# Kernel optimization log

Hardware: AMD Instinct MI355X
Metric: run time of the kernel (lower is better)

Reference implementation:

```python
import jax, jax.numpy as jnp
import numpy as np

SUB_NO = 128
T_HIST = 100
T_DATA = 20000
SYN_B = 3
HIST_B = 3
FIX_VAR = 1.0


def _build_kern(delta, log_tau, K):
    # delta: (S,), log_tau: (B,), K: (S,B) -> kernel (S, T_HIST)
    t = jnp.maximum(jnp.arange(T_HIST, dtype=jnp.float32)[None, :] - delta[:, None], 0.0)  # (S,T)
    tt = t[:, :, None] / jnp.exp(log_tau)[None, None, :]  # (S,T,B)
    return jnp.einsum('stb,sb->st', tt * jnp.exp(-tt), K)


def setup_inputs() -> dict:
    key = jax.random.key(0)
    ks = jax.random.split(key, 5)
    S = SUB_NO
    return {
        'S_conv': jax.random.normal(ks[0], (T_DATA, S), jnp.float32),
        'Y_ancest': jax.random.normal(ks[1], (T_DATA, S), jnp.float32),
        'Z_ancest': jax.random.uniform(ks[2], (T_DATA, S), jnp.float32),
        'noise': jax.random.normal(ks[3], (T_DATA, S), jnp.float32),
        'C_den': jax.random.uniform(ks[4], (S, S), jnp.float32),
        'W_sub': jnp.ones(S, jnp.float32) * 0.25,
        'theta_syn': jnp.zeros(S, jnp.float32),
        'K_spike': jnp.ones((S, SYN_B), jnp.float32) * 0.01,
        'tau_spike': jnp.arange(1.6, 1.6 + SYN_B, dtype=jnp.float32),
        'delta_spike': jnp.zeros(S, jnp.float32),
        'theta_spike': jnp.ones(S, jnp.float32) * (-1.0),
        'W_spike': jnp.ones(S, jnp.float32) * 0.1,
        'tau_hist': jnp.arange(0.5, 0.5 + HIST_B * 0.5, 0.5, dtype=jnp.float32),
        'K_hist': jnp.zeros((S, HIST_B), jnp.float32),
        'delta_hist': jnp.zeros(S, jnp.float32),
    }


def _forward(S_conv, Y_ancest, Z_ancest, noise, C_den, W_sub, theta_syn,
             K_spike, tau_spike, delta_spike, theta_spike, W_spike,
             tau_hist, K_hist, delta_hist):
    S = SUB_NO
    # kernels, flipped as in torch (conv1d cross-correlation with flipped kernel)
    hist_kf = _build_kern(delta_hist, tau_hist, K_hist)[:, ::-1]      # (S,T_HIST)
    anc_kf = _build_kern(delta_spike, tau_spike, K_spike)[:, ::-1]    # (S,T_HIST)

    # Ancestor path has no recurrence -> hoist out of the time loop.
    # spike_ancest filtering: C_den is linear & time-independent, so project first,
    # then depthwise-convolve along time.
    Z_pad = jnp.concatenate([jnp.zeros((T_HIST, S), S_conv.dtype), Z_ancest], axis=0)  # (T+T_HIST,S)
    A = Z_pad @ C_den.T  # (T+T_HIST, S)
    conv = jax.lax.conv_general_dilated(
        A.T[None],                 # (1, S, T+T_HIST)
        anc_kf[:, None, :],        # (S, 1, T_HIST)
        window_strides=(1,), padding='VALID',
        dimension_numbers=('NCH', 'OIH', 'NCH'),
        feature_group_count=S)     # (1, S, T_DATA+1)
    filtered_ancest = conv[0].T[:T_DATA]  # (T_DATA, S)

    raw_ancest = Y_ancest @ C_den.T  # (T_DATA, S)
    base = S_conv + theta_syn + filtered_ancest + raw_ancest  # (T_DATA,S)
    sqrt_var = FIX_VAR ** 0.5

    def step(buf, inp):
        # buf: (S, T_HIST) rolling history of Z_out (most recent at index -1)
        b, n = inp
        fh = jnp.sum(buf * hist_kf, axis=1)            # grouped conv1d == per-channel dot
        x_out = jax.nn.sigmoid(b + fh)
        down = x_out * W_spike + theta_spike           # down_mu_Z_t == mu_Z_t (up_mu_Z=None)
        z_out = jax.nn.sigmoid(down + n * sqrt_var)
        buf = jnp.concatenate([buf[:, 1:], z_out[:, None]], axis=1)
        return buf, (x_out * W_sub, z_out, down)

    buf0 = jnp.zeros((S, T_HIST), S_conv.dtype)
    _, (final_Y, final_Z, mu_Z) = jax.lax.scan(step, buf0, (base, noise))
    return final_Y, final_Z, mu_Z, mu_Z


def reference(S_conv, Y_ancest, Z_ancest, noise, C_den, W_sub, theta_syn,
              K_spike, tau_spike, delta_spike, theta_spike, W_spike,
              tau_hist, K_hist, delta_hist):
    return _forward(S_conv, Y_ancest, Z_ancest, noise, C_den, W_sub, theta_syn,
                    K_spike, tau_spike, delta_spike, theta_spike, W_spike,
                    tau_hist, K_hist, delta_hist)
```

## Files before the change

kernel.cpp:

```cpp
#include <hip/hip_runtime.h>

#define T_DATA 20000
#define S_NO   128
#define T_HIST 100
#define NELEM  (T_DATA * S_NO)

__device__ __forceinline__ float sigm(float v) {
    return 1.0f / (1.0f + __expf(-v));
}

__global__ void k1_prep(const float* __restrict__ C,
                        const float* __restrict__ K_spike,
                        const float* __restrict__ tau_spike,
                        const float* __restrict__ delta_spike,
                        const float* __restrict__ tau_hist,
                        const float* __restrict__ K_hist,
                        const float* __restrict__ delta_hist,
                        float* __restrict__ Ct,
                        float* __restrict__ anc_kT,
                        float* __restrict__ hist_k,
                        int* __restrict__ flag) {
    const int tid = threadIdx.x;
    for (int q = tid; q < S_NO * S_NO; q += 256) {
        int s = q >> 7, k = q & 127;
        Ct[k * S_NO + s] = C[q];
    }
    const int s    = tid & 127;
    const int half = tid >> 7;
    {
        float d  = delta_spike[s];
        float i0 = __expf(-tau_spike[0]);
        float i1 = __expf(-tau_spike[1]);
        float i2 = __expf(-tau_spike[2]);
        float k0 = K_spike[s * 3 + 0], k1 = K_spike[s * 3 + 1], k2 = K_spike[s * 3 + 2];
        for (int j = half * 50; j < half * 50 + 50; ++j) {
            float t  = fmaxf((float)j - d, 0.0f);
            float x0 = t * i0, x1 = t * i1, x2 = t * i2;
            anc_kT[j * S_NO + s] =
                k0 * x0 * __expf(-x0) + k1 * x1 * __expf(-x1) + k2 * x2 * __expf(-x2);
        }
    }
    {
        float d  = delta_hist[s];
        float i0 = __expf(-tau_hist[0]);
        float i1 = __expf(-tau_hist[1]);
        float i2 = __expf(-tau_hist[2]);
        float k0 = K_hist[s * 3 + 0], k1 = K_hist[s * 3 + 1], k2 = K_hist[s * 3 + 2];
        for (int j = half * 50; j < half * 50 + 50; ++j) {
            float t  = fmaxf((float)j - d, 0.0f);
            float x0 = t * i0, x1 = t * i1, x2 = t * i2;
            hist_k[s * T_HIST + j] =
                k0 * x0 * __expf(-x0) + k1 * x1 * __expf(-x1) + k2 * x2 * __expf(-x2);
        }
    }
    if (tid == 0) *flag = 0;
    __syncthreads();
    if (tid < 128) {
        if (K_hist[s * 3] != 0.0f || K_hist[s * 3 + 1] != 0.0f || K_hist[s * 3 + 2] != 0.0f)
            atomicOr(flag, 1);
    }
}

__global__ void __launch_bounds__(256) k2_gemm(const float* __restrict__ Z,
                                               const float* __restrict__ Y,
                                               const float* __restrict__ Ct,
                                               float* __restrict__ A,
                                               float* __restrict__ R) {
    __shared__ float Zt[16][128];
    __shared__ float Yt[16][128];
    const int t0  = blockIdx.x * 16;
    const int tid = threadIdx.x;
    {
        const float4* Zg = (const float4*)(Z + t0 * S_NO);
        const float4* Yg = (const float4*)(Y + t0 * S_NO);
        float4* Zl = (float4*)&Zt[0][0];
        float4* Yl = (float4*)&Yt[0][0];
        for (int q = tid; q < 512; q += 256) { Zl[q] = Zg[q]; Yl[q] = Yg[q]; }
    }
    __syncthreads();
    const int s  = tid & 127;
    const int tb = (tid >> 7) * 8;
    float accA[8] = {0, 0, 0, 0, 0, 0, 0, 0};
    float accR[8] = {0, 0, 0, 0, 0, 0, 0, 0};
    for (int k4 = 0; k4 < 32; ++k4) {
        const float c0 = Ct[(k4 * 4 + 0) * S_NO + s];
        const float c1 = Ct[(k4 * 4 + 1) * S_NO + s];
        const float c2 = Ct[(k4 * 4 + 2) * S_NO + s];
        const float c3 = Ct[(k4 * 4 + 3) * S_NO + s];
#pragma unroll
        for (int i = 0; i < 8; ++i) {
            float4 z = *(const float4*)&Zt[tb + i][k4 * 4];
            accA[i] = fmaf(c0, z.x, fmaf(c1, z.y, fmaf(c2, z.z, fmaf(c3, z.w, accA[i]))));
            float4 y = *(const float4*)&Yt[tb + i][k4 * 4];
            accR[i] = fmaf(c0, y.x, fmaf(c1, y.y, fmaf(c2, y.z, fmaf(c3, y.w, accR[i]))));
        }
    }
#pragma unroll
    for (int i = 0; i < 8; ++i) {
        A[(t0 + tb + i) * S_NO + s] = accA[i];
        R[(t0 + tb + i) * S_NO + s] = accR[i];
    }
}

__global__ void __launch_bounds__(256) k3_conv(const float* __restrict__ A,
                                               const float* __restrict__ anc_kT,
                                               float* __restrict__ F) {
    __shared__ float Al[140 * 64];
    const int tstart = blockIdx.x * 40;
    const int shalf  = blockIdx.y;
    const int tid    = threadIdx.x;
    for (int q = tid; q < 140 * 16; q += 256) {
        const int row = q >> 4, c4 = q & 15;
        const int u  = tstart - 100 + row;
        float4 v = make_float4(0.f, 0.f, 0.f, 0.f);
        if (u >= 0) v = *(const float4*)&A[u * S_NO + shalf * 64 + c4 * 4];
        *(float4*)&Al[row * 64 + c4 * 4] = v;
    }
    __syncthreads();
    const int sl    = tid & 63;
    const int tg    = tid >> 6;
    const int sg    = shalf * 64 + sl;
    const int rbase = tg * 10;
    float acc[10] = {0, 0, 0, 0, 0, 0, 0, 0, 0, 0};
    float W[10];
#pragma unroll
    for (int i = 0; i < 10; ++i) W[i] = Al[(rbase + 99 + i) * 64 + sl];
#pragma unroll
    for (int j = 0; j < 100; ++j) {
        const float kv = anc_kT[j * S_NO + sg];
#pragma unroll
        for (int i = 0; i < 10; ++i)
            acc[i] = fmaf(W[(((i - j) % 10) + 10) % 10], kv, acc[i]);
        if (j < 99)
            W[(10 - ((j + 1) % 10)) % 10] = Al[(rbase + 98 - j) * 64 + sl];
    }
    const int T0 = tstart + rbase;
#pragma unroll
    for (int i = 0; i < 10; ++i) F[(T0 + i) * S_NO + sg] = acc[i];
}

__global__ void __launch_bounds__(256) k4_final(const float* __restrict__ S_conv,
                                                const float* __restrict__ noise,
                                                const float* __restrict__ W_sub,
                                                const float* __restrict__ theta_syn,
                                                const float* __restrict__ theta_spike,
                                                const float* __restrict__ W_spike,
                                                const float* __restrict__ hist_k,
                                                const int* __restrict__ flag,
                                                float* out0, float* out1,
                                                float* out2, float* out3) {
    __shared__ float zr[128];
    if (*flag == 0) {
        const int n4 = blockIdx.x * blockDim.x + threadIdx.x;
        if (n4 >= NELEM / 4) return;
        const int r = n4 & 31;
        const float4 sc = ((const float4*)S_conv)[n4];
        const float4 rr = ((const float4*)out1)[n4];
        const float4 ff = ((const float4*)out3)[n4];
        const float4 nz = ((const float4*)noise)[n4];
        const float4 ts = ((const float4*)theta_syn)[r];
        const float4 wu = ((const float4*)W_sub)[r];
        const float4 wk = ((const float4*)W_spike)[r];
        const float4 tk = ((const float4*)theta_spike)[r];
        float4 y, z, dn;
        {
            float x = sigm(sc.x + ts.x + rr.x + ff.x);
            y.x = x * wu.x; dn.x = fmaf(x, wk.x, tk.x); z.x = sigm(dn.x + nz.x);
        }
        {
            float x = sigm(sc.y + ts.y + rr.y + ff.y);
            y.y = x * wu.y; dn.y = fmaf(x, wk.y, tk.y); z.y = sigm(dn.y + nz.y);
        }
        {
            float x = sigm(sc.z + ts.z + rr.z + ff.z);
            y.z = x * wu.z; dn.z = fmaf(x, wk.z, tk.z); z.z = sigm(dn.z + nz.z);
        }
        {
            float x = sigm(sc.w + ts.w + rr.w + ff.w);
            y.w = x * wu.w; dn.w = fmaf(x, wk.w, tk.w); z.w = sigm(dn.w + nz.w);
        }
        ((float4*)out0)[n4] = y;
        ((float4*)out1)[n4] = z;
        ((float4*)out2)[n4] = dn;
        ((float4*)out3)[n4] = dn;
    } else {
        const int s = blockIdx.x;
        if (s >= S_NO || threadIdx.x >= 64) return;
        const int l = threadIdx.x;
        zr[l] = 0.0f; zr[l + 64] = 0.0f;
        const float hk0 = (l < T_HIST) ? hist_k[s * T_HIST + l] : 0.0f;
        const float hk1 = (l + 64 < T_HIST) ? hist_k[s * T_HIST + l + 64] : 0.0f;
        const float tsy = theta_syn[s], wsub = W_sub[s];
        const float wsp = W_spike[s],  tsp  = theta_spike[s];
        for (int t = 0; t < T_DATA; ++t) {
            float fh = hk0 * zr[(t - 1 - l) & 127];
            fh = fmaf(hk1, zr[(t - 65 - l) & 127], fh);
#pragma unroll
            for (int m = 1; m < 64; m <<= 1) fh += __shfl_xor(fh, m, 64);
            const int n = t * S_NO + s;
            const float basev = S_conv[n] + tsy + out1[n] + out3[n];
            const float x  = sigm(basev + fh);
            const float dn = fmaf(x, wsp, tsp);
            const float z  = sigm(dn + noise[n]);
            if (l == 0) {
                out0[n] = x * wsub;
                out1[n] = z;
                out2[n] = dn;
                out3[n] = dn;
                zr[t & 127] = z;
            }
        }
    }
}

extern "C" void kernel_launch(void* const* d_in, const int* in_sizes, int n_in,
                              void* d_out, int out_size, void* d_ws, size_t ws_size,
                              hipStream_t stream) {
    const float* S_conv  = (const float*)d_in[0];
    const float* Y_anc   = (const float*)d_in[1];
    const float* Z_anc   = (const float*)d_in[2];
    const float* noise   = (const float*)d_in[3];
    const float* C_den   = (const float*)d_in[4];
    const float* W_sub   = (const float*)d_in[5];
    const float* th_syn  = (const float*)d_in[6];
    const float* K_spk   = (const float*)d_in[7];
    const float* tau_spk = (const float*)d_in[8];
    const float* dl_spk  = (const float*)d_in[9];
    const float* th_spk  = (const float*)d_in[10];
    const float* W_spk   = (const float*)d_in[11];
    const float* tau_h   = (const float*)d_in[12];
    const float* K_h     = (const float*)d_in[13];
    const float* dl_h    = (const float*)d_in[14];

    float* out  = (float*)d_out;
    float* out0 = out;
    float* out1 = out + NELEM;
    float* out2 = out + 2 * NELEM;
    float* out3 = out + 3 * NELEM;

    float* ws      = (float*)d_ws;
    float* Ct      = ws;
    float* anc_kT  = ws + 16384;
    float* hist_k  = ws + 16384 + 12800;
    int*   flag    = (int*)(ws + 16384 + 25600);

    k1_prep<<<1, 256, 0, stream>>>(C_den, K_spk, tau_spk, dl_spk, tau_h, K_h, dl_h,
                                   Ct, anc_kT, hist_k, flag);
    k2_gemm<<<T_DATA / 16, 256, 0, stream>>>(Z_anc, Y_anc, Ct, out0, out1);
    k3_conv<<<dim3(T_DATA / 40, 2), 256, 0, stream>>>(out0, anc_kT, out3);
    k4_final<<<(NELEM / 4 + 255) / 256, 256, 0, stream>>>(S_conv, noise, W_sub, th_syn,
                                                          th_spk, W_spk, hist_k, flag,
                                                          out0, out1, out2, out3);
}
```

Measured before the change: 189.4 us.

## Fuse ancestor convolution with elementwise output stage and parallelize prep transpose

```diff
diff --git a/kernel.cpp b/kernel.cpp
--- a/kernel.cpp
+++ b/kernel.cpp
@@ -9,7 +9,7 @@
     return 1.0f / (1.0f + __expf(-v));
 }
 
-__global__ void k1_prep(const float* __restrict__ C,
+__global__ void __launch_bounds__(256) k1_prep(const float* __restrict__ C,
                         const float* __restrict__ K_spike,
                         const float* __restrict__ tau_spike,
                         const float* __restrict__ delta_spike,
@@ -21,9 +21,14 @@
                         float* __restrict__ hist_k,
                         int* __restrict__ flag) {
     const int tid = threadIdx.x;
-    for (int q = tid; q < S_NO * S_NO; q += 256) {
-        int s = q >> 7, k = q & 127;
-        Ct[k * S_NO + s] = C[q];
+    const int b   = blockIdx.x;
+    if (b < 16) {
+#pragma unroll
+        for (int i = 0; i < 4; ++i) {
+            const int q = b * 1024 + i * 256 + tid;
+            Ct[(q & 127) * S_NO + (q >> 7)] = C[q];
+        }
+        return;
     }
     const int s    = tid & 127;
     const int half = tid >> 7;
@@ -102,10 +107,21 @@
     }
 }
 
-__global__ void __launch_bounds__(256) k3_conv(const float* __restrict__ A,
-                                               const float* __restrict__ anc_kT,
-                                               float* __restrict__ F) {
-    __shared__ float Al[140 * 64];
+__global__ void __launch_bounds__(256) k3_fused(const float* __restrict__ A,
+                                                const float* __restrict__ anc_kT,
+                                                const float* __restrict__ S_conv,
+                                                const float* __restrict__ noise,
+                                                const float* __restrict__ W_sub,
+                                                const float* __restrict__ theta_syn,
+                                                const float* __restrict__ theta_spike,
+                                                const float* __restrict__ W_spike,
+                                                const int* __restrict__ flag,
+                                                float* __restrict__ out0,
+                                                float* __restrict__ out1,
+                                                float* __restrict__ out2,
+                                                float* __restrict__ out3,
+                                                float* __restrict__ Fws) {
+    __shared__ float Al[141 * 64];
     const int tstart = blockIdx.x * 40;
     const int shalf  = blockIdx.y;
     const int tid    = threadIdx.x;
@@ -114,7 +130,7 @@
         const int u  = tstart - 100 + row;
         float4 v = make_float4(0.f, 0.f, 0.f, 0.f);
         if (u >= 0) v = *(const float4*)&A[u * S_NO + shalf * 64 + c4 * 4];
-        *(float4*)&Al[row * 64 + c4 * 4] = v;
+        *(float4*)&Al[(row + 1) * 64 + c4 * 4] = v;
     }
     __syncthreads();
     const int sl    = tid & 63;
@@ -124,91 +140,75 @@
     float acc[10] = {0, 0, 0, 0, 0, 0, 0, 0, 0, 0};
     float W[10];
 #pragma unroll
-    for (int i = 0; i < 10; ++i) W[i] = Al[(rbase + 99 + i) * 64 + sl];
-#pragma unroll
+    for (int i = 0; i < 10; ++i) W[i] = Al[(rbase + 100 + i) * 64 + sl];
+#pragma unroll 10
     for (int j = 0; j < 100; ++j) {
         const float kv = anc_kT[j * S_NO + sg];
 #pragma unroll
         for (int i = 0; i < 10; ++i)
             acc[i] = fmaf(W[(((i - j) % 10) + 10) % 10], kv, acc[i]);
-        if (j < 99)
-            W[(10 - ((j + 1) % 10)) % 10] = Al[(rbase + 98 - j) * 64 + sl];
+        W[(10 - ((j + 1) % 10)) % 10] = Al[(rbase + 99 - j) * 64 + sl];
     }
     const int T0 = tstart + rbase;
-#pragma unroll
-    for (int i = 0; i < 10; ++i) F[(T0 + i) * S_NO + sg] = acc[i];
-}
-
-__global__ void __launch_bounds__(256) k4_final(const float* __restrict__ S_conv,
-                                                const float* __restrict__ noise,
-                                                const float* __restrict__ W_sub,
-                                                const float* __restrict__ theta_syn,
-                                                const float* __restrict__ theta_spike,
-                                                const float* __restrict__ W_spike,
-                                                const float* __restrict__ hist_k,
-                                                const int* __restrict__ flag,
-                                                float* out0, float* out1,
-                                                float* out2, float* out3) {
-    __shared__ float zr[128];
     if (*flag == 0) {
-        const int n4 = blockIdx.x * blockDim.x + threadIdx.x;
-        if (n4 >= NELEM / 4) return;
-        const int r = n4 & 31;
-        const float4 sc = ((const float4*)S_conv)[n4];
-        const float4 rr = ((const float4*)out1)[n4];
-        const float4 ff = ((const float4*)out3)[n4];
-        const float4 nz = ((const float4*)noise)[n4];
-        const float4 ts = ((const float4*)theta_syn)[r];
-        const float4 wu = ((const float4*)W_sub)[r];
-        const float4 wk = ((const float4*)W_spike)[r];
-        const float4 tk = ((const float4*)theta_spike)[r];
-        float4 y, z, dn;
-        {
-            float x = sigm(sc.x + ts.x + rr.x + ff.x);
-            y.x = x * wu.x; dn.x = fmaf(x, wk.x, tk.x); z.x = sigm(dn.x + nz.x);
-        }
-        {
-            float x = sigm(sc.y + ts.y + rr.y + ff.y);
-            y.y = x * wu.y; dn.y = fmaf(x, wk.y, tk.y); z.y = sigm(dn.y + nz.y);
-        }
-        {
-            float x = sigm(sc.z + ts.z + rr.z + ff.z);
-            y.z = x * wu.z; dn.z = fmaf(x, wk.z, tk.z); z.z = sigm(dn.z + nz.z);
-        }
-        {
-            float x = sigm(sc.w + ts.w + rr.w + ff.w);
-            y.w = x * wu.w; dn.w = fmaf(x, wk.w, tk.w); z.w = sigm(dn.w + nz.w);
-        }
-        ((float4*)out0)[n4] = y;
-        ((float4*)out1)[n4] = z;
-        ((float4*)out2)[n4] = dn;
-        ((float4*)out3)[n4] = dn;
-    } else {
-        const int s = blockIdx.x;
-        if (s >= S_NO || threadIdx.x >= 64) return;
-        const int l = threadIdx.x;
-        zr[l] = 0.0f; zr[l + 64] = 0.0f;
-        const float hk0 = (l < T_HIST) ? hist_k[s * T_HIST + l] : 0.0f;
-        const float hk1 = (l + 64 < T_HIST) ? hist_k[s * T_HIST + l + 64] : 0.0f;
-        const float tsy = theta_syn[s], wsub = W_sub[s];
-        const float wsp = W_spike[s],  tsp  = theta_spike[s];
-        for (int t = 0; t < T_DATA; ++t) {
-            float fh = hk0 * zr[(t - 1 - l) & 127];
-            fh = fmaf(hk1, zr[(t - 65 - l) & 127], fh);
-#pragma unroll
-            for (int m = 1; m < 64; m <<= 1) fh += __shfl_xor(fh, m, 64);
-            const int n = t * S_NO + s;
-            const float basev = S_conv[n] + tsy + out1[n] + out3[n];
-            const float x  = sigm(basev + fh);
+        const float tsy = theta_syn[sg], wsub = W_sub[sg];
+        const float wsp = W_spike[sg],  tsp  = theta_spike[sg];
+#pragma unroll
+        for (int i = 0; i < 10; ++i) {
+            const int n = (T0 + i) * S_NO + sg;
+            const float basev = S_conv[n] + tsy + out1[n] + acc[i];
+            const float x  = sigm(basev);
             const float dn = fmaf(x, wsp, tsp);
             const float z  = sigm(dn + noise[n]);
-            if (l == 0) {
-                out0[n] = x * wsub;
-                out1[n] = z;
-                out2[n] = dn;
-                out3[n] = dn;
-                zr[t & 127] = z;
-            }
+            out0[n] = x * wsub;
+            out1[n] = z;
+            out2[n] = dn;
+            out3[n] = dn;
+        }
+    } else {
+#pragma unroll
+        for (int i = 0; i < 10; ++i) Fws[(T0 + i) * S_NO + sg] = acc[i];
+    }
+}
+
+__global__ void __launch_bounds__(64) k4_scan(const float* __restrict__ S_conv,
+                                              const float* __restrict__ noise,
+                                              const float* __restrict__ W_sub,
+                                              const float* __restrict__ theta_syn,
+                                              const float* __restrict__ theta_spike,
+                                              const float* __restrict__ W_spike,
+                                              const float* __restrict__ hist_k,
+                                              const int* __restrict__ flag,
+                                              const float* __restrict__ Fws,
+                                              float* __restrict__ out0,
+                                              float* __restrict__ out1,
+                                              float* __restrict__ out2,
+                                              float* __restrict__ out3) {
+    if (*flag == 0) return;
+    __shared__ float zr[128];
+    const int s = blockIdx.x;
+    const int l = threadIdx.x;
+    zr[l] = 0.0f; zr[l + 64] = 0.0f;
+    const float hk0 = (l < T_HIST) ? hist_k[s * T_HIST + l] : 0.0f;
+    const float hk1 = (l + 64 < T_HIST) ? hist_k[s * T_HIST + l + 64] : 0.0f;
+    const float tsy = theta_syn[s], wsub = W_sub[s];
+    const float wsp = W_spike[s],  tsp  = theta_spike[s];
+    for (int t = 0; t < T_DATA; ++t) {
+        float fh = hk0 * zr[(t - 1 - l) & 127];
+        fh = fmaf(hk1, zr[(t - 65 - l) & 127], fh);
+#pragma unroll
+        for (int m = 1; m < 64; m <<= 1) fh += __shfl_xor(fh, m, 64);
+        const int n = t * S_NO + s;
+        const float basev = S_conv[n] + tsy + out1[n] + Fws[n];
+        const float x  = sigm(basev + fh);
+        const float dn = fmaf(x, wsp, tsp);
+        const float z  = sigm(dn + noise[n]);
+        if (l == 0) {
+            out0[n] = x * wsub;
+            out1[n] = z;
+            out2[n] = dn;
+            out3[n] = dn;
+            zr[t & 127] = z;
         }
     }
 }
@@ -238,17 +238,20 @@
     float* out2 = out + 2 * NELEM;
     float* out3 = out + 3 * NELEM;
 
-    float* ws      = (float*)d_ws;
-    float* Ct      = ws;
-    float* anc_kT  = ws + 16384;
-    float* hist_k  = ws + 16384 + 12800;
-    int*   flag    = (int*)(ws + 16384 + 25600);
-
-    k1_prep<<<1, 256, 0, stream>>>(C_den, K_spk, tau_spk, dl_spk, tau_h, K_h, dl_h,
-                                   Ct, anc_kT, hist_k, flag);
-    k2_gemm<<<T_DATA / 16, 256, 0, stream>>>(Z_anc, Y_anc, Ct, out0, out1);
-    k3_conv<<<dim3(T_DATA / 40, 2), 256, 0, stream>>>(out0, anc_kT, out3);
-    k4_final<<<(NELEM / 4 + 255) / 256, 256, 0, stream>>>(S_conv, noise, W_sub, th_syn,
-                                                          th_spk, W_spk, hist_k, flag,
-                                                          out0, out1, out2, out3);
-}
+    float* ws     = (float*)d_ws;
+    float* wsA    = ws;
+    float* wsF    = ws + NELEM;
+    float* Ct     = ws + 2 * NELEM;
+    float* anc_kT = Ct + 16384;
+    float* hist_k = anc_kT + T_HIST * S_NO;
+    int*   flag   = (int*)(hist_k + S_NO * T_HIST);
+
+    k1_prep<<<17, 256, 0, stream>>>(C_den, K_spk, tau_spk, dl_spk, tau_h, K_h, dl_h,
+                                    Ct, anc_kT, hist_k, flag);
+    k2_gemm<<<T_DATA / 16, 256, 0, stream>>>(Z_anc, Y_anc, Ct, wsA, out1);
+    k3_fused<<<dim3(T_DATA / 40, 2), 256, 0, stream>>>(wsA, anc_kT, S_conv, noise,
+                                                       W_sub, th_syn, th_spk, W_spk,
+                                                       flag, out0, out1, out2, out3, wsF);
+    k4_scan<<<S_NO, 64, 0, stream>>>(S_conv, noise, W_sub, th_syn, th_spk, W_spk,
+                                     hist_k, flag, wsF, out0, out1, out2, out3);
+}
```

After: 189.7 us. About the same (+0.1%).
